# Optimization experiments

Hardware: AMD Instinct MI355X
Metric: run time of the kernel (lower is better)

## Reference

```python
import jax, jax.numpy as jnp
import numpy as np

RADIUS = 51  # odd-ified from 50
WEIGHT = 0.5
THRESHOLD = 10.0


def _gaussian_kernel_2d(k: int) -> np.ndarray:
    # Replicates cv2.getGaussianKernel(k, 0): sigma = 0.3*((k-1)*0.5 - 1) + 0.8
    sigma = 0.3 * ((k - 1) * 0.5 - 1.0) + 0.8
    x = np.arange(k, dtype=np.float64) - (k - 1) / 2.0
    g = np.exp(-(x ** 2) / (2.0 * sigma ** 2))
    g = g / g.sum()
    return np.outer(g, g).astype(np.float32)  # (k, k)


def filter2d(img, kernel):
    # img: (b, c, h, w), kernel: (k, k); depthwise 'same' conv (symmetric zero pad)
    b, c, h, w = img.shape
    k = kernel.shape[-1]
    p = k // 2
    x = img.reshape(b * c, 1, h, w)
    w2 = kernel.reshape(1, 1, k, k).astype(img.dtype)
    out = jax.lax.conv_general_dilated(
        x, w2,
        window_strides=(1, 1),
        padding=[(p, p), (p, p)],
        dimension_numbers=("NCHW", "OIHW", "NCHW"),
    )
    return out.reshape(b, c, h, w)


def setup_inputs() -> dict:
    key = jax.random.key(0)
    img = jax.random.uniform(key, (16, 3, 512, 512), dtype=jnp.float32)
    kernel = jnp.asarray(_gaussian_kernel_2d(RADIUS))
    return {"img": img, "kernel": kernel}


def reference(img, kernel):
    blur = filter2d(img, kernel)
    residual = img - blur
    mask = (jnp.abs(residual) * 255.0 > THRESHOLD).astype(img.dtype)
    soft_mask = filter2d(mask, kernel)
    sharp = jnp.clip(img + WEIGHT * residual, 0.0, 1.0)
    return soft_mask * sharp + (1.0 - soft_mask) * img
```

## Files before the change

### kernel.cpp

```cpp
#include <hip/hip_runtime.h>
#include <hip/hip_fp16.h>
#include <math.h>

#define IMG_H 512
#define IMG_W 512
#define NCH   48
#define KR    51
#define PAD   25
#define PADL  28
#define ROWW  568
#define WEIGHT 0.5f
#define THRESH 10.0f

typedef float f32x4 __attribute__((ext_vector_type(4)));

struct GK { float g[KR]; };

__device__ __forceinline__ int swz6144(int b) { return (b & 7) * 768 + (b >> 3); }

__device__ __forceinline__ void hblur4(const float* tl, int t, const GK& gk,
                                       float a[4]) {
  a[0] = a[1] = a[2] = a[3] = 0.f;
  #pragma unroll
  for (int m = 0; m < 15; ++m) {
    float4 q = *reinterpret_cast<const float4*>(&tl[4 * t + 4 * m]);
    float qa[4] = {q.x, q.y, q.z, q.w};
    #pragma unroll
    for (int e = 0; e < 4; ++e)
      #pragma unroll
      for (int o = 0; o < 4; ++o) {
        int j = 4 * m + e - o - 3;
        if (j >= 0 && j < KR) a[o] += gk.g[j] * qa[e];
      }
  }
}

template <bool CHK>
__device__ __forceinline__ void vacc4(const __half* p , int y0,
                                      const GK& gk, float acc[4][4]) {
  #pragma unroll
  for (int u = 0; u < 4; ++u)
    acc[u][0] = acc[u][1] = acc[u][2] = acc[u][3] = 0.f;
  #pragma unroll
  for (int d = -PAD; d <= 3 + PAD; ++d) {
    int ry = y0 + d;
    if (CHK && ((unsigned)ry >= (unsigned)IMG_H)) continue;
    union { uint2 u2; __half2 h[2]; } pk;
    pk.u2 = *reinterpret_cast<const uint2*>(p + (size_t)ry * IMG_W);
    float q0 = __low2float(pk.h[0]), q1 = __high2float(pk.h[0]);
    float q2 = __low2float(pk.h[1]), q3 = __high2float(pk.h[1]);
    #pragma unroll
    for (int u = 0; u < 4; ++u) {
      int j = d - u + PAD;
      if (j >= 0 && j < KR) {
        float w = gk.g[j];
        acc[u][0] += w * q0; acc[u][1] += w * q1;
        acc[u][2] += w * q2; acc[u][3] += w * q3;
      }
    }
  }
}

__global__ __launch_bounds__(256, 8) void k1_hblur(const float* __restrict__ in,
                                                   __half* __restrict__ out, GK gk) {
  __shared__ float tile[2][ROWW];
  const int tid = threadIdx.x;
  const int sub = tid >> 7;
  const int t   = tid & 127;
  const int row = blockIdx.x * 2 + sub;
  const float* rin = in + (size_t)row * IMG_W;
  float* tl = tile[sub];
  float4 v = *reinterpret_cast<const float4*>(&rin[4 * t]);
  if (t < 28) { tl[t] = 0.f; tl[PADL + 512 + t] = 0.f; }
  *reinterpret_cast<float4*>(&tl[PADL + 4 * t]) = v;
  __syncthreads();
  float a[4];
  hblur4(tl, t, gk, a);
  union { uint2 u2; __half2 h[2]; } pk;
  pk.h[0] = __floats2half2_rn(a[0], a[1]);
  pk.h[1] = __floats2half2_rn(a[2], a[3]);
  *reinterpret_cast<uint2*>(&out[(size_t)row * IMG_W + 4 * t]) = pk.u2;
}

__global__ __launch_bounds__(128, 6) void k2_vres_hmask(
    const __half* __restrict__ t1, const float* __restrict__ img,
    __half* __restrict__ res, __half* __restrict__ t2, GK gk) {
  const int t  = threadIdx.x;
  const int l  = swz6144(blockIdx.x);
  const int yb = l & 127;
  const int c  = l >> 7;
  const int y0 = yb * 4;
  const int x  = 4 * t;
  const size_t base = (size_t)c * IMG_H * IMG_W;
  float acc[4][4];
  if (y0 >= PADL && y0 + 3 + PADL < IMG_H)
    vacc4<false>(t1 + base + x, y0, gk, acc);
  else
    vacc4<true>(t1 + base + x, y0, gk, acc);

  __shared__ float tl[4][ROWW];
  for (int i = t; i < 224; i += 128) {
    int u = i / 56, k = i % 56;
    tl[u][k < 28 ? k : 512 + k] = 0.f;
  }
  #pragma unroll
  for (int u = 0; u < 4; ++u) {
    const size_t off = base + (size_t)(y0 + u) * IMG_W + x;
    float4 iv = *reinterpret_cast<const float4*>(&img[off]);
    float r0 = iv.x - acc[u][0], r1 = iv.y - acc[u][1];
    float r2 = iv.z - acc[u][2], r3 = iv.w - acc[u][3];
    union { uint2 u2; __half2 h[2]; } pk;
    pk.h[0] = __floats2half2_rn(r0, r1);
    pk.h[1] = __floats2half2_rn(r2, r3);
    *reinterpret_cast<uint2*>(&res[off]) = pk.u2;
    float m0 = (fabsf(r0) * 255.f > THRESH) ? 1.f : 0.f;
    float m1 = (fabsf(r1) * 255.f > THRESH) ? 1.f : 0.f;
    float m2 = (fabsf(r2) * 255.f > THRESH) ? 1.f : 0.f;
    float m3 = (fabsf(r3) * 255.f > THRESH) ? 1.f : 0.f;
    *reinterpret_cast<float4*>(&tl[u][PADL + x]) =
        make_float4(m0, m1, m2, m3);
  }
  __syncthreads();
  #pragma unroll
  for (int u = 0; u < 4; ++u) {
    float a[4];
    hblur4(tl[u], t, gk, a);
    union { uint2 u2; __half2 h[2]; } pk;
    pk.h[0] = __floats2half2_rn(a[0], a[1]);
    pk.h[1] = __floats2half2_rn(a[2], a[3]);
    *reinterpret_cast<uint2*>(&t2[base + (size_t)(y0 + u) * IMG_W + x]) = pk.u2;
  }
}

__global__ __launch_bounds__(128, 6) void k3_vfinal(
    const __half* __restrict__ t2, const float* __restrict__ img,
    const __half* __restrict__ res, float* __restrict__ out, GK gk) {
  const int t  = threadIdx.x;
  const int l  = swz6144(blockIdx.x);
  const int yb = l & 127;
  const int c  = l >> 7;
  const int y0 = yb * 4;
  const int x  = 4 * t;
  const size_t base = (size_t)c * IMG_H * IMG_W;
  float acc[4][4];
  if (y0 >= PADL && y0 + 3 + PADL < IMG_H)
    vacc4<false>(t2 + base + x, y0, gk, acc);
  else
    vacc4<true>(t2 + base + x, y0, gk, acc);

  #pragma unroll
  for (int u = 0; u < 4; ++u) {
    const size_t off = base + (size_t)(y0 + u) * IMG_W + x;
    float4 iv = *reinterpret_cast<const float4*>(&img[off]);
    union { uint2 u2; __half2 h[2]; } pk;
    pk.u2 = *reinterpret_cast<const uint2*>(&res[off]);
    float r[4]  = { __low2float(pk.h[0]), __high2float(pk.h[0]),
                    __low2float(pk.h[1]), __high2float(pk.h[1]) };
    float iva[4] = { iv.x, iv.y, iv.z, iv.w };
    float o[4];
    #pragma unroll
    for (int e = 0; e < 4; ++e) {
      float sharp = fminf(fmaxf(iva[e] + WEIGHT * r[e], 0.f), 1.f);
      o[e] = iva[e] + acc[u][e] * (sharp - iva[e]);
    }
    f32x4 ov = { o[0], o[1], o[2], o[3] };
    __builtin_nontemporal_store(ov, reinterpret_cast<f32x4*>(&out[off]));
  }
}

extern "C" void kernel_launch(void* const* d_in, const int* in_sizes, int n_in,
                              void* d_out, int out_size, void* d_ws, size_t ws_size,
                              hipStream_t stream) {
  const float* img = (const float*)d_in[0];
  GK gk;
  {
    double sigma = 0.3 * ((KR - 1) * 0.5 - 1.0) + 0.8;
    double gs[KR], sum = 0.0;
    for (int i = 0; i < KR; ++i) {
      double xd = (double)i - (KR - 1) / 2.0;
      gs[i] = exp(-(xd * xd) / (2.0 * sigma * sigma));
      sum += gs[i];
    }
    for (int i = 0; i < KR; ++i) gk.g[i] = (float)(gs[i] / sum);
  }

  const size_t npx = (size_t)NCH * IMG_H * IMG_W;
  __half* tmp1 = (__half*)d_out;
  __half* res  = (__half*)d_ws;
  __half* tmp2 = (__half*)((char*)d_ws + npx * sizeof(__half));

  const int hblocks = NCH * IMG_H / 2;
  const int vblocks = NCH * (IMG_H / 4);

  k1_hblur     <<<hblocks, 256, 0, stream>>>(img, tmp1, gk);
  k2_vres_hmask<<<vblocks, 128, 0, stream>>>(tmp1, img, res, tmp2, gk);
  k3_vfinal    <<<vblocks, 128, 0, stream>>>(tmp2, img, res, (float*)d_out, gk);
}
```

Before: 239.2 us.

## Widen per-thread work to 8 columns across all three blur kernels

Each thread now computes 8 horizontal outputs instead of 4, using 16-byte fp16 loads in the vertical passes and a wider horizontal register blur. Block sizes are halved so the grid shape stays the same, and the launch-bound occupancy hints change. The nontemporal output store is replaced by plain stores, and the interior/boundary check now uses PAD instead of PADL. The goal is more reuse per loaded value and fewer memory instructions, at the cost of higher register pressure and fewer threads per block.

```diff
diff --git a/kernel.cpp b/kernel.cpp
--- a/kernel.cpp
+++ b/kernel.cpp
@@ -12,23 +12,22 @@
 #define WEIGHT 0.5f
 #define THRESH 10.0f
 
-typedef float f32x4 __attribute__((ext_vector_type(4)));
-
 struct GK { float g[KR]; };
 
 __device__ __forceinline__ int swz6144(int b) { return (b & 7) * 768 + (b >> 3); }
 
-__device__ __forceinline__ void hblur4(const float* tl, int t, const GK& gk,
-                                       float a[4]) {
-  a[0] = a[1] = a[2] = a[3] = 0.f;
-  #pragma unroll
-  for (int m = 0; m < 15; ++m) {
-    float4 q = *reinterpret_cast<const float4*>(&tl[4 * t + 4 * m]);
+__device__ __forceinline__ void hblur8(const float* tl, int t, const GK& gk,
+                                       float a[8]) {
+  #pragma unroll
+  for (int o = 0; o < 8; ++o) a[o] = 0.f;
+  #pragma unroll
+  for (int m = 0; m < 16; ++m) {
+    float4 q = *reinterpret_cast<const float4*>(&tl[8 * t + 4 * m]);
     float qa[4] = {q.x, q.y, q.z, q.w};
     #pragma unroll
     for (int e = 0; e < 4; ++e)
       #pragma unroll
-      for (int o = 0; o < 4; ++o) {
+      for (int o = 0; o < 8; ++o) {
         int j = 4 * m + e - o - 3;
         if (j >= 0 && j < KR) a[o] += gk.g[j] * qa[e];
       }
@@ -36,53 +35,61 @@
 }
 
 template <bool CHK>
-__device__ __forceinline__ void vacc4(const __half* p , int y0,
-                                      const GK& gk, float acc[4][4]) {
+__device__ __forceinline__ void vacc8(const __half* p , int y0,
+                                      const GK& gk, float acc[4][8]) {
   #pragma unroll
   for (int u = 0; u < 4; ++u)
-    acc[u][0] = acc[u][1] = acc[u][2] = acc[u][3] = 0.f;
+    #pragma unroll
+    for (int k = 0; k < 8; ++k) acc[u][k] = 0.f;
   #pragma unroll
   for (int d = -PAD; d <= 3 + PAD; ++d) {
     int ry = y0 + d;
     if (CHK && ((unsigned)ry >= (unsigned)IMG_H)) continue;
-    union { uint2 u2; __half2 h[2]; } pk;
-    pk.u2 = *reinterpret_cast<const uint2*>(p + (size_t)ry * IMG_W);
-    float q0 = __low2float(pk.h[0]), q1 = __high2float(pk.h[0]);
-    float q2 = __low2float(pk.h[1]), q3 = __high2float(pk.h[1]);
+    uint4 raw = *reinterpret_cast<const uint4*>(p + (size_t)ry * IMG_W);
+    const __half* h = reinterpret_cast<const __half*>(&raw);
     #pragma unroll
     for (int u = 0; u < 4; ++u) {
       int j = d - u + PAD;
       if (j >= 0 && j < KR) {
         float w = gk.g[j];
-        acc[u][0] += w * q0; acc[u][1] += w * q1;
-        acc[u][2] += w * q2; acc[u][3] += w * q3;
+        #pragma unroll
+        for (int k = 0; k < 8; ++k)
+          acc[u][k] = fmaf(__half2float(h[k]), w, acc[u][k]);
       }
     }
   }
 }
 
-__global__ __launch_bounds__(256, 8) void k1_hblur(const float* __restrict__ in,
+__device__ __forceinline__ uint4 pack8(const float a[8]) {
+  union { uint4 u4; __half2 h[4]; } pk;
+  pk.h[0] = __floats2half2_rn(a[0], a[1]);
+  pk.h[1] = __floats2half2_rn(a[2], a[3]);
+  pk.h[2] = __floats2half2_rn(a[4], a[5]);
+  pk.h[3] = __floats2half2_rn(a[6], a[7]);
+  return pk.u4;
+}
+
+__global__ __launch_bounds__(128, 5) void k1_hblur(const float* __restrict__ in,
                                                    __half* __restrict__ out, GK gk) {
   __shared__ float tile[2][ROWW];
   const int tid = threadIdx.x;
-  const int sub = tid >> 7;
-  const int t   = tid & 127;
+  const int sub = tid >> 6;
+  const int t   = tid & 63;
   const int row = blockIdx.x * 2 + sub;
   const float* rin = in + (size_t)row * IMG_W;
   float* tl = tile[sub];
-  float4 v = *reinterpret_cast<const float4*>(&rin[4 * t]);
+  float4 v0 = *reinterpret_cast<const float4*>(&rin[8 * t]);
+  float4 v1 = *reinterpret_cast<const float4*>(&rin[8 * t + 4]);
   if (t < 28) { tl[t] = 0.f; tl[PADL + 512 + t] = 0.f; }
-  *reinterpret_cast<float4*>(&tl[PADL + 4 * t]) = v;
+  *reinterpret_cast<float4*>(&tl[PADL + 8 * t])     = v0;
+  *reinterpret_cast<float4*>(&tl[PADL + 8 * t + 4]) = v1;
   __syncthreads();
-  float a[4];
-  hblur4(tl, t, gk, a);
-  union { uint2 u2; __half2 h[2]; } pk;
-  pk.h[0] = __floats2half2_rn(a[0], a[1]);
-  pk.h[1] = __floats2half2_rn(a[2], a[3]);
-  *reinterpret_cast<uint2*>(&out[(size_t)row * IMG_W + 4 * t]) = pk.u2;
-}
-
-__global__ __launch_bounds__(128, 6) void k2_vres_hmask(
+  float a[8];
+  hblur8(tl, t, gk, a);
+  *reinterpret_cast<uint4*>(&out[(size_t)row * IMG_W + 8 * t]) = pack8(a);
+}
+
+__global__ __launch_bounds__(64, 5) void k2_vres_hmask(
     const __half* __restrict__ t1, const float* __restrict__ img,
     __half* __restrict__ res, __half* __restrict__ t2, GK gk) {
   const int t  = threadIdx.x;
@@ -90,49 +97,47 @@
   const int yb = l & 127;
   const int c  = l >> 7;
   const int y0 = yb * 4;
-  const int x  = 4 * t;
+  const int x  = 8 * t;
   const size_t base = (size_t)c * IMG_H * IMG_W;
-  float acc[4][4];
-  if (y0 >= PADL && y0 + 3 + PADL < IMG_H)
-    vacc4<false>(t1 + base + x, y0, gk, acc);
+  float acc[4][8];
+  if (y0 >= PAD && y0 + 3 + PAD < IMG_H)
+    vacc8<false>(t1 + base + x, y0, gk, acc);
   else
-    vacc4<true>(t1 + base + x, y0, gk, acc);
+    vacc8<true>(t1 + base + x, y0, gk, acc);
 
   __shared__ float tl[4][ROWW];
-  for (int i = t; i < 224; i += 128) {
+  for (int i = t; i < 224; i += 64) {
     int u = i / 56, k = i % 56;
     tl[u][k < 28 ? k : 512 + k] = 0.f;
   }
   #pragma unroll
   for (int u = 0; u < 4; ++u) {
     const size_t off = base + (size_t)(y0 + u) * IMG_W + x;
-    float4 iv = *reinterpret_cast<const float4*>(&img[off]);
-    float r0 = iv.x - acc[u][0], r1 = iv.y - acc[u][1];
-    float r2 = iv.z - acc[u][2], r3 = iv.w - acc[u][3];
-    union { uint2 u2; __half2 h[2]; } pk;
-    pk.h[0] = __floats2half2_rn(r0, r1);
-    pk.h[1] = __floats2half2_rn(r2, r3);
-    *reinterpret_cast<uint2*>(&res[off]) = pk.u2;
-    float m0 = (fabsf(r0) * 255.f > THRESH) ? 1.f : 0.f;
-    float m1 = (fabsf(r1) * 255.f > THRESH) ? 1.f : 0.f;
-    float m2 = (fabsf(r2) * 255.f > THRESH) ? 1.f : 0.f;
-    float m3 = (fabsf(r3) * 255.f > THRESH) ? 1.f : 0.f;
+    float4 iv0 = *reinterpret_cast<const float4*>(&img[off]);
+    float4 iv1 = *reinterpret_cast<const float4*>(&img[off + 4]);
+    float ia[8] = {iv0.x, iv0.y, iv0.z, iv0.w, iv1.x, iv1.y, iv1.z, iv1.w};
+    float r[8], m[8];
+    #pragma unroll
+    for (int k = 0; k < 8; ++k) {
+      r[k] = ia[k] - acc[u][k];
+      m[k] = (fabsf(r[k]) * 255.f > THRESH) ? 1.f : 0.f;
+    }
+    *reinterpret_cast<uint4*>(&res[off]) = pack8(r);
     *reinterpret_cast<float4*>(&tl[u][PADL + x]) =
-        make_float4(m0, m1, m2, m3);
+        make_float4(m[0], m[1], m[2], m[3]);
+    *reinterpret_cast<float4*>(&tl[u][PADL + x + 4]) =
+        make_float4(m[4], m[5], m[6], m[7]);
   }
   __syncthreads();
   #pragma unroll
   for (int u = 0; u < 4; ++u) {
-    float a[4];
-    hblur4(tl[u], t, gk, a);
-    union { uint2 u2; __half2 h[2]; } pk;
-    pk.h[0] = __floats2half2_rn(a[0], a[1]);
-    pk.h[1] = __floats2half2_rn(a[2], a[3]);
-    *reinterpret_cast<uint2*>(&t2[base + (size_t)(y0 + u) * IMG_W + x]) = pk.u2;
-  }
-}
-
-__global__ __launch_bounds__(128, 6) void k3_vfinal(
+    float a[8];
+    hblur8(tl[u], t, gk, a);
+    *reinterpret_cast<uint4*>(&t2[base + (size_t)(y0 + u) * IMG_W + x]) = pack8(a);
+  }
+}
+
+__global__ __launch_bounds__(64, 5) void k3_vfinal(
     const __half* __restrict__ t2, const float* __restrict__ img,
     const __half* __restrict__ res, float* __restrict__ out, GK gk) {
   const int t  = threadIdx.x;
@@ -140,31 +145,32 @@
   const int yb = l & 127;
   const int c  = l >> 7;
   const int y0 = yb * 4;
-  const int x  = 4 * t;
+  const int x  = 8 * t;
   const size_t base = (size_t)c * IMG_H * IMG_W;
-  float acc[4][4];
-  if (y0 >= PADL && y0 + 3 + PADL < IMG_H)
-    vacc4<false>(t2 + base + x, y0, gk, acc);
+  float acc[4][8];
+  if (y0 >= PAD && y0 + 3 + PAD < IMG_H)
+    vacc8<false>(t2 + base + x, y0, gk, acc);
   else
-    vacc4<true>(t2 + base + x, y0, gk, acc);
+    vacc8<true>(t2 + base + x, y0, gk, acc);
 
   #pragma unroll
   for (int u = 0; u < 4; ++u) {
     const size_t off = base + (size_t)(y0 + u) * IMG_W + x;
-    float4 iv = *reinterpret_cast<const float4*>(&img[off]);
-    union { uint2 u2; __half2 h[2]; } pk;
-    pk.u2 = *reinterpret_cast<const uint2*>(&res[off]);
-    float r[4]  = { __low2float(pk.h[0]), __high2float(pk.h[0]),
-                    __low2float(pk.h[1]), __high2float(pk.h[1]) };
-    float iva[4] = { iv.x, iv.y, iv.z, iv.w };
-    float o[4];
-    #pragma unroll
-    for (int e = 0; e < 4; ++e) {
-      float sharp = fminf(fmaxf(iva[e] + WEIGHT * r[e], 0.f), 1.f);
-      o[e] = iva[e] + acc[u][e] * (sharp - iva[e]);
-    }
-    f32x4 ov = { o[0], o[1], o[2], o[3] };
-    __builtin_nontemporal_store(ov, reinterpret_cast<f32x4*>(&out[off]));
+    float4 iv0 = *reinterpret_cast<const float4*>(&img[off]);
+    float4 iv1 = *reinterpret_cast<const float4*>(&img[off + 4]);
+    uint4 rr = *reinterpret_cast<const uint4*>(&res[off]);
+    const __half* rh = reinterpret_cast<const __half*>(&rr);
+    float ia[8] = {iv0.x, iv0.y, iv0.z, iv0.w, iv1.x, iv1.y, iv1.z, iv1.w};
+    float o[8];
+    #pragma unroll
+    for (int k = 0; k < 8; ++k) {
+      float sharp = fminf(fmaxf(fmaf(WEIGHT, __half2float(rh[k]), ia[k]), 0.f), 1.f);
+      o[k] = fmaf(acc[u][k], sharp - ia[k], ia[k]);
+    }
+    *reinterpret_cast<float4*>(&out[off]) =
+        make_float4(o[0], o[1], o[2], o[3]);
+    *reinterpret_cast<float4*>(&out[off + 4]) =
+        make_float4(o[4], o[5], o[6], o[7]);
   }
 }
 
@@ -192,7 +198,7 @@
   const int hblocks = NCH * IMG_H / 2;
   const int vblocks = NCH * (IMG_H / 4);
 
-  k1_hblur     <<<hblocks, 256, 0, stream>>>(img, tmp1, gk);
-  k2_vres_hmask<<<vblocks, 128, 0, stream>>>(tmp1, img, res, tmp2, gk);
-  k3_vfinal    <<<vblocks, 128, 0, stream>>>(tmp2, img, res, (float*)d_out, gk);
-}
+  k1_hblur     <<<hblocks, 128, 0, stream>>>(img, tmp1, gk);
+  k2_vres_hmask<<<vblocks,  64, 0, stream>>>(tmp1, img, res, tmp2, gk);
+  k3_vfinal    <<<vblocks,  64, 0, stream>>>(tmp2, img, res, (float*)d_out, gk);
+}
```

Measured after the change: 632.0 us. +164.2%, slower.
